# Optimization experiments

Hardware: AMD Instinct MI355X
Metric: run time of the kernel (lower is better)

Reference implementation:

```python
import jax, jax.numpy as jnp
import numpy as np
from jax import lax

# ---- geometry (from Mamba2PoSTMixer defaults + chosen d_model) ----
D_MODEL = 1024
EXPAND = 2
HEADDIM = 64
D_STATE = 128
D_CONV = 4
CHUNK = 256
D_INNER = EXPAND * D_MODEL            # 2048
NHEADS = D_INNER // HEADDIM           # 32
D_CONV_CH = D_INNER + 2 * D_STATE     # conv acts on x, B, C
D_IN_PROJ = 2 * D_INNER + 2 * D_STATE + NHEADS
BATCH, SEQLEN = 2, 4096
EPS = 1e-5


def setup_inputs() -> dict:
    key = jax.random.key(0)
    ks = jax.random.split(key, 8)
    f = jnp.float32
    return {
        "hidden_states": jax.random.normal(ks[0], (BATCH, SEQLEN, D_MODEL), f),
        "residual": jax.random.normal(ks[1], (BATCH, SEQLEN, D_MODEL), f),
        "norm_weight": jnp.ones((D_MODEL,), f),
        "in_proj_w": jax.random.normal(ks[2], (D_MODEL, D_IN_PROJ), f) * 0.02,
        "conv_w": jax.random.normal(ks[3], (D_CONV, 1, D_CONV_CH), f) * 0.2,  # WIO, depthwise
        "conv_b": jnp.zeros((D_CONV_CH,), f),
        "dt_bias": jnp.log(jnp.expm1(jax.random.uniform(ks[4], (NHEADS,), f, 1e-3, 1e-1))),
        "A_log": jnp.log(jax.random.uniform(ks[5], (NHEADS,), f, 1.0, 16.0)),
        "D": jnp.ones((NHEADS,), f),
        "gate_norm_weight": jnp.ones((D_INNER,), f),
        "out_proj_w": jax.random.normal(ks[6], (D_INNER, D_MODEL), f) * 0.02,
    }


def _rmsnorm(x, w, eps=EPS):
    return x * lax.rsqrt(jnp.mean(x * x, axis=-1, keepdims=True) + eps) * w


def _segsum(x):
    # x: [..., T] -> [..., T, T] lower-triangular cumulative segment sums
    T = x.shape[-1]
    cs = jnp.cumsum(x, axis=-1)
    ss = cs[..., :, None] - cs[..., None, :]
    mask = jnp.tril(jnp.ones((T, T), bool))
    return jnp.where(mask, ss, -jnp.inf)


def _ssd(xdt, dtA, Bm, Cm):
    # xdt: [b,l,h,p] (x already scaled by dt), dtA: [b,l,h], Bm/Cm: [b,l,n]
    b, l, h, p = xdt.shape
    n = Bm.shape[-1]
    c = l // CHUNK
    x = xdt.reshape(b, c, CHUNK, h, p)
    A = dtA.reshape(b, c, CHUNK, h).transpose(0, 3, 1, 2)     # [b,h,c,l]
    Bc = Bm.reshape(b, c, CHUNK, n)
    Cc = Cm.reshape(b, c, CHUNK, n)
    A_cum = jnp.cumsum(A, axis=-1)                            # [b,h,c,l]
    # intra-chunk (diagonal block) output
    L = jnp.exp(_segsum(A))                                   # [b,h,c,l,s]
    Y_diag = jnp.einsum('bcln,bcsn,bhcls,bcshp->bclhp', Cc, Bc, L, x)
    # per-chunk final states
    decay_states = jnp.exp(A_cum[..., -1:] - A_cum)           # [b,h,c,l]
    states = jnp.einsum('bcln,bhcl,bclhp->bchpn', Bc, decay_states, x)
    # inter-chunk recurrence over chunk states
    chunk_decay = jnp.exp(A_cum[..., -1])                     # [b,h,c]
    def step(carry, inp):
        dec, s = inp                                          # dec: [b,h], s: [b,h,p,n]
        return carry * dec[..., None, None] + s, carry
    init = jnp.zeros((b, h, p, n), xdt.dtype)
    _, prev = lax.scan(step, init,
                       (jnp.moveaxis(chunk_decay, -1, 0), jnp.moveaxis(states, 1, 0)))
    prev = jnp.moveaxis(prev, 0, 1)                           # [b,c,h,p,n] states entering each chunk
    Y_off = jnp.einsum('bcln,bchpn,bhcl->bclhp', Cc, prev, jnp.exp(A_cum))
    return (Y_diag + Y_off).reshape(b, l, h, p)


def reference(hidden_states, residual, norm_weight, in_proj_w, conv_w, conv_b,
              dt_bias, A_log, D, gate_norm_weight, out_proj_w):
    # residual add + RMSNorm (Mamba2PoSTBlock)
    res = hidden_states + residual
    h = _rmsnorm(res, norm_weight)
    # Mamba2 mixer
    zxbcdt = h @ in_proj_w                                    # [b,l, 2*Di + 2*N + H]
    z, xBC, dt_raw = jnp.split(zxbcdt, [D_INNER, D_INNER + D_CONV_CH], axis=-1)
    # depthwise causal conv over (x, B, C) channels + SiLU
    xp = jnp.pad(xBC, ((0, 0), (D_CONV - 1, 0), (0, 0)))
    xBC = lax.conv_general_dilated(xp, conv_w, (1,), 'VALID',
                                   dimension_numbers=('NWC', 'WIO', 'NWC'),
                                   feature_group_count=D_CONV_CH) + conv_b
    xBC = jax.nn.silu(xBC)
    x, Bm, Cm = jnp.split(xBC, [D_INNER, D_INNER + D_STATE], axis=-1)
    dt = jax.nn.softplus(dt_raw + dt_bias)                    # [b,l,H]
    A = -jnp.exp(A_log)                                       # [H]
    xh = x.reshape(x.shape[0], x.shape[1], NHEADS, HEADDIM)   # [b,l,h,p]
    y = _ssd(xh * dt[..., None], dt * A, Bm, Cm)
    y = y + D[None, None, :, None] * xh                       # skip (D) term
    y = y.reshape(y.shape[0], y.shape[1], D_INNER)
    y = _rmsnorm(y * jax.nn.silu(z), gate_norm_weight)        # gated RMSNorm
    out = y @ out_proj_w
    return out, res
```

## Files before the change

kernel.cpp:

```cpp
#include <hip/hip_runtime.h>
#include <hip/hip_bf16.h>
#include <math.h>

#define BATCH   2
#define LQ      4096
#define RTOT    8192
#define DM      1024
#define DI      2048
#define NH      32
#define HD      64
#define DS      128
#define CH      256
#define NC      16
#define XBC_C   2304
#define ZX_C    4384
#define ZXS     4352
#define NP1     4608
#define EPS     1e-5f
#define LOG2E   1.4426950408889634f

typedef __hip_bfloat16 bf16;
typedef __bf16 bf16x8v __attribute__((ext_vector_type(8)));
typedef __bf16 bf16x4v __attribute__((ext_vector_type(4)));
typedef float f32x4v __attribute__((ext_vector_type(4)));

__device__ __forceinline__ float block_reduce_sum(float v) {
    __shared__ float sred[8];
    int lane = threadIdx.x & 63, w = threadIdx.x >> 6;
#pragma unroll
    for (int off = 32; off > 0; off >>= 1) v += __shfl_down(v, off, 64);
    if (lane == 0) sred[w] = v;
    __syncthreads();
    float t = (threadIdx.x < (int)(blockDim.x >> 6)) ? sred[threadIdx.x] : 0.f;
    if (w == 0) {
#pragma unroll
        for (int off = 4; off > 0; off >>= 1) t += __shfl_down(t, off, 64);
        if (lane == 0) sred[0] = t;
    }
    __syncthreads();
    return sred[0];
}

__device__ __forceinline__ void transpose_tile(
    const float* __restrict__ W, bf16* __restrict__ WT, int K, int N,
    int n0, int k0) {
    __shared__ float t[32][33];
    int tx = threadIdx.x & 31, ty = threadIdx.x >> 5;
#pragma unroll
    for (int r = 0; r < 32; r += 8) {
        int k = k0 + ty + r, n = n0 + tx;
        t[ty + r][tx] = (n < N) ? W[(size_t)k * N + n] : 0.f;
    }
    __syncthreads();
#pragma unroll
    for (int r = 0; r < 32; r += 8) {
        int n = n0 + ty + r, k = k0 + tx;
        WT[(size_t)n * K + k] = __float2bfloat16(t[tx][ty + r]);
    }
}

__global__ __launch_bounds__(256) void fused_pre_kernel(
    const float* __restrict__ hid, const float* __restrict__ resid,
    const float* __restrict__ w, float* __restrict__ res_out,
    bf16* __restrict__ h_out, const float* __restrict__ in_proj,
    bf16* __restrict__ Bt1) {
    int bid = blockIdx.x;
    if (bid < RTOT) {
        int r = bid, tid = threadIdx.x;
        size_t base = (size_t)r * DM;
        float4 hv = *(const float4*)&hid[base + tid * 4];
        float4 rv = *(const float4*)&resid[base + tid * 4];
        float4 s = {hv.x + rv.x, hv.y + rv.y, hv.z + rv.z, hv.w + rv.w};
        *(float4*)&res_out[base + tid * 4] = s;
        float ss = s.x * s.x + s.y * s.y + s.z * s.z + s.w * s.w;
        ss = block_reduce_sum(ss);
        float scale = rsqrtf(ss / (float)DM + EPS);
        float4 wv = *(const float4*)&w[tid * 4];
        __hip_bfloat162 p0, p1;
        p0.x = __float2bfloat16(s.x * scale * wv.x);
        p0.y = __float2bfloat16(s.y * scale * wv.y);
        p1.x = __float2bfloat16(s.z * scale * wv.z);
        p1.y = __float2bfloat16(s.w * scale * wv.w);
        bf16* hp = &h_out[base + tid * 4];
        *(__hip_bfloat162*)hp = p0;
        *(__hip_bfloat162*)(hp + 2) = p1;
    } else {
        int t = bid - RTOT;
        transpose_tile(in_proj, Bt1, DM, ZX_C, (t % 144) * 32, (t / 144) * 32);
    }
}

#define GFENCE asm volatile("" ::: "memory")
#define GBAR do { GFENCE; __builtin_amdgcn_s_barrier(); GFENCE; } while (0)
#define GWAIT_LGKM                                                             \
    do {                                                                       \
        asm volatile("s_waitcnt lgkmcnt(0)" ::: "memory");                     \
        __builtin_amdgcn_sched_barrier(0);                                     \
    } while (0)
#define GWAIT_VM0 asm volatile("s_waitcnt vmcnt(0)" ::: "memory")
#define GWAIT_VMN                                                              \
    do {                                                                       \
        if constexpr (BN == 256)                                               \
            asm volatile("s_waitcnt vmcnt(6)" ::: "memory");                   \
        else                                                                   \
            asm volatile("s_waitcnt vmcnt(4)" ::: "memory");                   \
    } while (0)

#define RD_A(buf, ml)                                                          \
    do {                                                                       \
        _Pragma("unroll") for (int mt_ = 0; mt_ < 4; ++mt_)                    \
        _Pragma("unroll") for (int kk_ = 0; kk_ < 2; ++kk_)                    \
            aF[mt_][kk_] = *(const bf16x8v*)&As[buf][                          \
                (wm * 128 + ((ml) * 4 + mt_) * 16 + fr) * 64 +                 \
                ((((kk_ << 2) | kg) ^ s7) << 3)];                              \
    } while (0)

#define RD_B(buf)                                                              \
    do {                                                                       \
        _Pragma("unroll") for (int nt_ = 0; nt_ < NTW; ++nt_)                  \
        _Pragma("unroll") for (int kk_ = 0; kk_ < 2; ++kk_)                    \
            bF[nt_][kk_] = *(const bf16x8v*)&Bs[buf][                          \
                (wn * (BN / 4) + nt_ * 16 + fr) * 64 +                         \
                ((((kk_ << 2) | kg) ^ s7) << 3)];                              \
    } while (0)

#define QMFMA(ml, nl)                                                          \
    do {                                                                       \
        __builtin_amdgcn_s_setprio(1);                                         \
        _Pragma("unroll") for (int mt_ = 0; mt_ < 4; ++mt_)                    \
        _Pragma("unroll") for (int nt_ = 0; nt_ < NTH; ++nt_)                  \
        _Pragma("unroll") for (int kk_ = 0; kk_ < 2; ++kk_)                    \
            acc[(ml) * 4 + mt_][(nl) * NTH + nt_] =                            \
                __builtin_amdgcn_mfma_f32_16x16x32_bf16(                       \
                    aF[mt_][kk_], bF[(nl) * NTH + nt_][kk_],                   \
                    acc[(ml) * 4 + mt_][(nl) * NTH + nt_], 0, 0, 0);           \
        __builtin_amdgcn_s_setprio(0);                                         \
    } while (0)

template <int BN, int WRITE_F32>
__global__ __launch_bounds__(512, 2) void gemm_8ph_kernel(
    const bf16* __restrict__ A, int lda, const bf16* __restrict__ Bt, int ldb,
    void* __restrict__ C, int ldc, int NXT, int K, float* __restrict__ dtraw) {
    constexpr int BM = 256;
    constexpr int NTW = BN / 64;
    constexpr int NTH = NTW / 2;
    constexpr int BLOADS = BN / 128;
    __shared__ __align__(16) bf16 As[2][BM * 64];
    __shared__ __align__(16) bf16 Bs[2][BN * 64];

    const int tid = threadIdx.x;
    const int lane = tid & 63;
    const int wave = tid >> 6;
    const int wm = wave >> 2, wn = wave & 3;
    const int fr = lane & 15, kg = lane >> 4;
    const int s7 = fr & 7;

    const int bid = blockIdx.x;
    const int swz = (bid & 7) * ((int)gridDim.x >> 3) + (bid >> 3);
    const int mtile = swz / NXT;
    const int m0 = mtile * BM;
    const int n0 = (swz - mtile * NXT) * BN;

    const int trow = tid >> 3;
    const int scol = ((tid & 7) ^ (trow & 7)) << 3;
    const bf16* aSrc = A + (size_t)(m0 + trow) * lda + scol;
    const bf16* bSrc = Bt + (size_t)(n0 + trow) * ldb + scol;

    auto stageA = [&](int kt, int h) {
#pragma unroll
        for (int j = 0; j < 2; ++j)
            __builtin_amdgcn_global_load_lds(
                (const __attribute__((address_space(1))) void*)(
                    aSrc + (size_t)(h * 128 + j * 64) * lda + kt * 64),
                (__attribute__((address_space(3))) void*)(
                    &As[kt & 1][(h * 128 + j * 64) * 64 + tid * 8]),
                16, 0, 0);
    };
    auto stageB = [&](int kt, int h) {
#pragma unroll
        for (int j = 0; j < BLOADS; ++j)
            __builtin_amdgcn_global_load_lds(
                (const __attribute__((address_space(1))) void*)(
                    bSrc + (size_t)(h * (BN / 2) + j * 64) * ldb + kt * 64),
                (__attribute__((address_space(3))) void*)(
                    &Bs[kt & 1][(h * (BN / 2) + j * 64) * 64 + tid * 8]),
                16, 0, 0);
    };

    f32x4v acc[8][NTW] = {};
    bf16x8v aF[4][2], bF[NTW][2];

    stageB(0, 0); stageB(0, 1); stageA(0, 0); stageA(0, 1);
    stageB(1, 0); stageB(1, 1); stageA(1, 0);
    GWAIT_VMN;
    GBAR;

    const int NIT = K >> 7;
    for (int t = 0; t < NIT; ++t) {
        const int k1 = 2 * t + 1, k2 = 2 * t + 2, k3 = 2 * t + 3;
        const bool full = (t < NIT - 1);
        RD_B(0); RD_A(0, 0);
        stageA(k1, 1);
        GBAR; GWAIT_LGKM;
        QMFMA(0, 0);
        GBAR;
        if (full) stageB(k2, 0);
        GBAR;
        QMFMA(0, 1);
        GBAR;
        RD_A(0, 1);
        if (full) stageB(k2, 1);
        GBAR; GWAIT_LGKM;
        QMFMA(1, 0);
        GBAR;
        if (full) stageA(k2, 0);
        GBAR;
        QMFMA(1, 1);
        if (full) { GWAIT_VMN; } else { GWAIT_VM0; }
        GBAR;
        RD_B(1); RD_A(1, 0);
        if (full) stageA(k2, 1);
        GBAR; GWAIT_LGKM;
        QMFMA(0, 0);
        GBAR;
        if (full) stageB(k3, 0);
        GBAR;
        QMFMA(0, 1);
        GBAR;
        RD_A(1, 1);
        if (full) stageB(k3, 1);
        GBAR; GWAIT_LGKM;
        QMFMA(1, 0);
        GBAR;
        if (full) stageA(k3, 0);
        GBAR;
        QMFMA(1, 1);
        if (full) { GWAIT_VMN; }
        GBAR;
    }

#pragma unroll
    for (int mt = 0; mt < 8; ++mt) {
#pragma unroll
        for (int nt = 0; nt < NTW; ++nt) {
            int gn = n0 + wn * (BN / 4) + nt * 16 + fr;
#pragma unroll
            for (int rg = 0; rg < 4; ++rg) {
                int gm = m0 + wm * 128 + mt * 16 + kg * 4 + rg;
                float v = acc[mt][nt][rg];
                if (WRITE_F32) {
                    ((float*)C)[(size_t)gm * ldc + gn] = v;
                } else {
                    if (gn < 4352)
                        ((bf16*)C)[(size_t)gm * ldc + gn] = __float2bfloat16(v);
                    else if (gn < 4384)
                        dtraw[(size_t)gm * 32 + (gn - 4352)] = v;
                }
            }
        }
    }
}

__global__ __launch_bounds__(256) void fused_conv_dt_kernel(
    const bf16* __restrict__ zx, const float* __restrict__ conv_w,
    const float* __restrict__ conv_b, bf16* __restrict__ xBC,
    const float* __restrict__ dtraw, const float* __restrict__ dt_bias,
    const float* __restrict__ A_log, float* __restrict__ dt_bh,
    float* __restrict__ Ac2_bh) {
    int bid = blockIdx.x;
    if (bid < 9216) {
        int idx = bid * 256 + threadIdx.x;
        int r = idx / 288;
        int o = idx - r * 288;
        int c = o * 8;
        int b = r >> 12, l = r & (LQ - 1);
        float acc[8];
        {
            float4 cb0 = *(const float4*)&conv_b[c];
            float4 cb1 = *(const float4*)&conv_b[c + 4];
            acc[0] = cb0.x; acc[1] = cb0.y; acc[2] = cb0.z; acc[3] = cb0.w;
            acc[4] = cb1.x; acc[5] = cb1.y; acc[6] = cb1.z; acc[7] = cb1.w;
        }
#pragma unroll
        for (int k = 0; k < 4; ++k) {
            int t = l - 3 + k;
            if (t >= 0) {
                bf16x8v xv = *(const bf16x8v*)&zx[(size_t)(b * LQ + t) * ZXS + DI + c];
                float4 w0 = *(const float4*)&conv_w[k * XBC_C + c];
                float4 w1 = *(const float4*)&conv_w[k * XBC_C + c + 4];
                acc[0] = fmaf(w0.x, (float)xv[0], acc[0]);
                acc[1] = fmaf(w0.y, (float)xv[1], acc[1]);
                acc[2] = fmaf(w0.z, (float)xv[2], acc[2]);
                acc[3] = fmaf(w0.w, (float)xv[3], acc[3]);
                acc[4] = fmaf(w1.x, (float)xv[4], acc[4]);
                acc[5] = fmaf(w1.y, (float)xv[5], acc[5]);
                acc[6] = fmaf(w1.z, (float)xv[6], acc[6]);
                acc[7] = fmaf(w1.w, (float)xv[7], acc[7]);
            }
        }
        bf16x8v ov;
#pragma unroll
        for (int j = 0; j < 8; ++j)
            ov[j] = (__bf16)(acc[j] / (1.f + __expf(-acc[j])));
        *(bf16x8v*)&xBC[(size_t)r * XBC_C + c] = ov;
    } else {
        __shared__ float sA[256];
        int b2 = bid - 9216;
        int c = b2 & 15, h = (b2 >> 4) & 31, b = b2 >> 9;
        int tid = threadIdx.x;
        int l = c * CH + tid;
        int r = b * LQ + l;
        float v = dtraw[(size_t)r * 32 + h] + dt_bias[h];
        float dt = (v > 20.f) ? v : log1pf(expf(v));
        float A = -expf(A_log[h]);
        sA[tid] = dt * A * LOG2E;
        __syncthreads();
        for (int off = 1; off < 256; off <<= 1) {
            float t = (tid >= off) ? sA[tid - off] : 0.f;
            __syncthreads();
            sA[tid] += t;
            __syncthreads();
        }
        size_t o = (size_t)(b * NH + h) * LQ + l;
        dt_bh[o] = dt;
        Ac2_bh[o] = sA[tid];
    }
}

__global__ __launch_bounds__(256) void states_mfma_kernel(
    const bf16* __restrict__ xBC, const float* __restrict__ dt_bh,
    const float* __restrict__ Ac2, float* __restrict__ states) {
    __shared__ __align__(16) __bf16 xdT[64][264];
    __shared__ __align__(16) __bf16 BT[64][264];
    int bid = blockIdx.x;
    int c = bid & 15, h = (bid >> 4) & 31, b = bid >> 9;
    int bh = b * NH + h;
    int rch = b * LQ + c * CH;
    int tid = threadIdx.x;
    int wave = tid >> 6, lane = tid & 63;
    int fr = lane & 15, kg = lane >> 4;
    float Ac2last = Ac2[(size_t)bh * LQ + c * CH + (CH - 1)];

    {
        int p2 = (tid & 31) * 2;
        int srow = tid >> 5;
#pragma unroll 4
        for (int pass = 0; pass < 32; ++pass) {
            int s = pass * 8 + srow;
            float sc = dt_bh[(size_t)bh * LQ + c * CH + s] *
                       exp2f(Ac2last - Ac2[(size_t)bh * LQ + c * CH + s]);
            __hip_bfloat162 xv =
                *(const __hip_bfloat162*)&xBC[(size_t)(rch + s) * XBC_C + h * HD + p2];
            xdT[p2][s]     = (__bf16)(__bfloat162float(xv.x) * sc);
            xdT[p2 + 1][s] = (__bf16)(__bfloat162float(xv.y) * sc);
        }
    }
    int wm = (wave >> 1) * 32, wn = (wave & 1) * 32;
    size_t base = (size_t)(bh * NC + c) * HD * DS;
    for (int nh = 0; nh < 2; ++nh) {
        __syncthreads();
        {
            int n_oct = tid & 7, lrow = tid >> 3;
#pragma unroll
            for (int pass = 0; pass < 8; ++pass) {
                int l = pass * 32 + lrow;
                bf16x8v bv = *(const bf16x8v*)
                    &xBC[(size_t)(rch + l) * XBC_C + DI + nh * 64 + n_oct * 8];
#pragma unroll
                for (int j = 0; j < 8; ++j)
                    BT[n_oct * 8 + j][l] = bv[j];
            }
        }
        __syncthreads();
        f32x4v acc[2][2] = {};
#pragma unroll
        for (int kb = 0; kb < 8; ++kb) {
            bf16x8v A2[2], B2[2];
#pragma unroll
            for (int i = 0; i < 2; ++i)
                A2[i] = *(const bf16x8v*)&xdT[wm + i * 16 + fr][kb * 32 + kg * 8];
#pragma unroll
            for (int j = 0; j < 2; ++j)
                B2[j] = *(const bf16x8v*)&BT[wn + j * 16 + fr][kb * 32 + kg * 8];
#pragma unroll
            for (int i = 0; i < 2; ++i)
#pragma unroll
                for (int j = 0; j < 2; ++j)
                    acc[i][j] = __builtin_amdgcn_mfma_f32_16x16x32_bf16(
                        A2[i], B2[j], acc[i][j], 0, 0, 0);
        }
#pragma unroll
        for (int i = 0; i < 2; ++i)
#pragma unroll
            for (int j = 0; j < 2; ++j)
#pragma unroll
                for (int rg = 0; rg < 4; ++rg) {
                    int p = wm + i * 16 + kg * 4 + rg;
                    int n = nh * 64 + wn + j * 16 + fr;
                    states[base + (size_t)p * DS + n] = acc[i][j][rg];
                }
    }
}

__global__ __launch_bounds__(256) void chunk_scan_kernel(
    float* __restrict__ states, const float* __restrict__ Ac2) {
    int bh = blockIdx.x;
    int tid = threadIdx.x;
    float carry[32];
#pragma unroll
    for (int j = 0; j < 32; ++j) carry[j] = 0.f;
    for (int c = 0; c < NC; ++c) {
        float dec = exp2f(Ac2[(size_t)bh * LQ + c * CH + (CH - 1)]);
        size_t base = (size_t)(bh * NC + c) * (HD * DS);
#pragma unroll
        for (int j = 0; j < 32; ++j) {
            size_t idx = base + tid + j * 256;
            float tmp = states[idx];
            states[idx] = carry[j];
            carry[j] = carry[j] * dec + tmp;
        }
    }
}

template <int MASKED>
__device__ __forceinline__ void y_slab(
    const bf16* __restrict__ xBC, int rch, int s0, int fr, int kg,
    const float* As_sh, const float* Al, const bf16x8v CA[4][4],
    __bf16 (*Pw)[36], const __bf16 (*xdtT)[264], f32x4v accY[4][4]) {
#pragma unroll
    for (int half = 0; half < 2; ++half) {
        f32x4v Sacc[2][4] = {};
#pragma unroll
        for (int ks = 0; ks < 4; ++ks) {
            bf16x8v SB[2];
#pragma unroll
            for (int st2 = 0; st2 < 2; ++st2)
                SB[st2] = *(const bf16x8v*)&xBC[
                    (size_t)(rch + s0 + half * 32 + st2 * 16 + fr) * XBC_C
                    + DI + ks * 32 + kg * 8];
#pragma unroll
            for (int st2 = 0; st2 < 2; ++st2)
#pragma unroll
                for (int mt = 0; mt < 4; ++mt) {
                    if (MASKED && (half * 2 + st2) > mt) continue;
                    Sacc[st2][mt] = __builtin_amdgcn_mfma_f32_16x16x32_bf16(
                        SB[st2], CA[mt][ks], Sacc[st2][mt], 0, 0, 0);
                }
        }
#pragma unroll
        for (int st2 = 0; st2 < 2; ++st2) {
            int sblk = half * 2 + st2;
            float4 As4 = *(const float4*)&As_sh[s0 + half * 32 + st2 * 16 + kg * 4];
            float as[4] = {As4.x, As4.y, As4.z, As4.w};
#pragma unroll
            for (int mt = 0; mt < 4; ++mt) {
                bf16x4v pv;
                if (MASKED && sblk > mt) {
                    pv[0] = pv[1] = pv[2] = pv[3] = (__bf16)0.f;
                } else {
#pragma unroll
                    for (int rg = 0; rg < 4; ++rg) {
                        float v = Sacc[st2][mt][rg] * exp2f(Al[mt] - as[rg]);
                        if (MASKED && sblk == mt && (kg * 4 + rg) > fr) v = 0.f;
                        pv[rg] = (__bf16)v;
                    }
                }
                *(bf16x4v*)&Pw[mt * 16 + fr][st2 * 16 + kg * 4] = pv;
            }
        }
        __asm__ volatile("s_waitcnt lgkmcnt(0)" ::: "memory");
        bf16x8v PA[4], XB[4];
#pragma unroll
        for (int mt = 0; mt < 4; ++mt) {
            bf16x4v plo = *(const bf16x4v*)&Pw[mt * 16 + fr][kg * 8];
            bf16x4v phi = *(const bf16x4v*)&Pw[mt * 16 + fr][kg * 8 + 4];
            bf16x8v pa;
#pragma unroll
            for (int j = 0; j < 4; ++j) { pa[j] = plo[j]; pa[4 + j] = phi[j]; }
            PA[mt] = pa;
        }
#pragma unroll
        for (int pt = 0; pt < 4; ++pt)
            XB[pt] = *(const bf16x8v*)&xdtT[pt * 16 + fr][s0 + half * 32 + kg * 8];
#pragma unroll
        for (int mt = 0; mt < 4; ++mt)
#pragma unroll
            for (int pt = 0; pt < 4; ++pt)
                accY[mt][pt] = __builtin_amdgcn_mfma_f32_16x16x32_bf16(
                    PA[mt], XB[pt], accY[mt][pt], 0, 0, 0);
        __asm__ volatile("s_waitcnt lgkmcnt(0)" ::: "memory");
    }
}

__global__ __launch_bounds__(256) void y_mfma_kernel(
    const bf16* __restrict__ xBC, const float* __restrict__ dt_bh,
    const float* __restrict__ Ac2, const float* __restrict__ prev,
    bf16* __restrict__ yout ) {
    __shared__ __align__(16) __bf16 xdtT[64][264];
    __shared__ __align__(16) __bf16 P[4][64][36];
    __shared__ float As_sh[256];
    int bid = blockIdx.x;
    int c = bid & 15, h = (bid >> 4) & 31, b = bid >> 9;
    int bh = b * NH + h;
    int rch = b * LQ + c * CH;
    int tid = threadIdx.x;
    int wave = tid >> 6, lane = tid & 63;
    int fr = lane & 15, kg = lane >> 4;

    As_sh[tid] = Ac2[(size_t)bh * LQ + c * CH + tid];
    {
        int p2 = (tid & 31) * 2;
        int srow = tid >> 5;
#pragma unroll 4
        for (int pass = 0; pass < 32; ++pass) {
            int s = pass * 8 + srow;
            float dtv = dt_bh[(size_t)bh * LQ + c * CH + s];
            __hip_bfloat162 xv =
                *(const __hip_bfloat162*)&xBC[(size_t)(rch + s) * XBC_C + h * HD + p2];
            xdtT[p2][s]     = (__bf16)(__bfloat162float(xv.x) * dtv);
            xdtT[p2 + 1][s] = (__bf16)(__bfloat162float(xv.y) * dtv);
        }
    }
    __syncthreads();

    bf16x8v CA[4][4];
    {
        size_t rb = (size_t)(rch + wave * 64 + fr) * XBC_C + DI + DS + kg * 8;
#pragma unroll
        for (int mt = 0; mt < 4; ++mt)
#pragma unroll
            for (int ks = 0; ks < 4; ++ks)
                CA[mt][ks] = *(const bf16x8v*)&xBC[rb + (size_t)mt * 16 * XBC_C + ks * 32];
    }

    f32x4v accY[4][4] = {};

    {
        size_t pbase = (size_t)(bh * NC + c) * HD * DS;
#pragma unroll
        for (int ks = 0; ks < 4; ++ks) {
            bf16x8v PB[4];
#pragma unroll
            for (int pt = 0; pt < 4; ++pt) {
                const float* pp = &prev[pbase + (size_t)(pt * 16 + fr) * DS + ks * 32 + kg * 8];
                float4 a4 = *(const float4*)pp;
                float4 b4 = *(const float4*)(pp + 4);
                bf16x8v t;
                t[0] = (__bf16)a4.x; t[1] = (__bf16)a4.y; t[2] = (__bf16)a4.z; t[3] = (__bf16)a4.w;
                t[4] = (__bf16)b4.x; t[5] = (__bf16)b4.y; t[6] = (__bf16)b4.z; t[7] = (__bf16)b4.w;
                PB[pt] = t;
            }
#pragma unroll
            for (int mt = 0; mt < 4; ++mt)
#pragma unroll
                for (int pt = 0; pt < 4; ++pt)
                    accY[mt][pt] = __builtin_amdgcn_mfma_f32_16x16x32_bf16(
                        CA[mt][ks], PB[pt], accY[mt][pt], 0, 0, 0);
        }
    }
    int l0 = wave * 64;
#pragma unroll
    for (int mt = 0; mt < 4; ++mt) {
#pragma unroll
        for (int rg = 0; rg < 4; ++rg) {
            float e = exp2f(As_sh[l0 + mt * 16 + kg * 4 + rg]);
#pragma unroll
            for (int pt = 0; pt < 4; ++pt)
                accY[mt][pt][rg] *= e;
        }
    }

    float Al[4];
#pragma unroll
    for (int mt = 0; mt < 4; ++mt) Al[mt] = As_sh[l0 + mt * 16 + fr];

    __bf16 (*Pw)[36] = P[wave];
    for (int st = 0; st < wave; ++st)
        y_slab<0>(xBC, rch, st * 64, fr, kg, As_sh, Al, CA, Pw, xdtT, accY);
    y_slab<1>(xBC, rch, l0, fr, kg, As_sh, Al, CA, Pw, xdtT, accY);

#pragma unroll
    for (int ph = 0; ph < 2; ++ph) {
#pragma unroll
        for (int mt = 0; mt < 4; ++mt)
#pragma unroll
            for (int ptl = 0; ptl < 2; ++ptl)
#pragma unroll
                for (int rg = 0; rg < 4; ++rg)
                    Pw[mt * 16 + kg * 4 + rg][ptl * 16 + fr] =
                        (__bf16)accY[mt][ph * 2 + ptl][rg];
        __asm__ volatile("s_waitcnt lgkmcnt(0)" ::: "memory");
        bf16* yp = yout + (size_t)(rch + l0 + lane) * ZXS + h * HD + ph * 32;
#pragma unroll
        for (int q = 0; q < 4; ++q) {
            bf16x4v a = *(const bf16x4v*)&Pw[lane][q * 8];
            bf16x4v bq = *(const bf16x4v*)&Pw[lane][q * 8 + 4];
            bf16x8v v;
#pragma unroll
            for (int j = 0; j < 4; ++j) { v[j] = a[j]; v[4 + j] = bq[j]; }
            *(bf16x8v*)(yp + q * 8) = v;
        }
        __asm__ volatile("s_waitcnt lgkmcnt(0)" ::: "memory");
    }
}

__global__ __launch_bounds__(256) void fused_gate_trans_kernel(
    const bf16* __restrict__ zx, const float* __restrict__ gw,
    const float* __restrict__ Dvec, const bf16* __restrict__ xBC,
    bf16* __restrict__ y ,
    const float* __restrict__ out_proj, bf16* __restrict__ Bt2) {
    int bid = blockIdx.x;
    if (bid < RTOT) {
        int r = bid, tid = threadIdx.x;
        int i0 = tid * 8;
        bf16x8v zv = *(const bf16x8v*)&zx[(size_t)r * ZXS + i0];
        bf16x8v yv = *(const bf16x8v*)&y[(size_t)r * ZXS + i0];
        bf16x8v xv = *(const bf16x8v*)&xBC[(size_t)r * XBC_C + i0];
        float Dh = Dvec[tid >> 3];
        float v[8];
        float ss = 0.f;
#pragma unroll
        for (int j = 0; j < 8; ++j) {
            float z = (float)zv[j];
            float val = ((float)yv[j] + Dh * (float)xv[j]) * (z / (1.f + __expf(-z)));
            v[j] = val;
            ss += val * val;
        }
        ss = block_reduce_sum(ss);
        float scale = rsqrtf(ss / (float)DI + EPS);
        float4 g0 = *(const float4*)&gw[i0];
        float4 g1 = *(const float4*)&gw[i0 + 4];
        float g[8] = {g0.x, g0.y, g0.z, g0.w, g1.x, g1.y, g1.z, g1.w};
        bf16x8v ov;
#pragma unroll
        for (int j = 0; j < 8; ++j)
            ov[j] = (__bf16)(v[j] * scale * g[j]);
        *(bf16x8v*)&y[(size_t)r * ZXS + i0] = ov;
    } else {
        int t = bid - RTOT;
        transpose_tile(out_proj, Bt2, DI, DM, (t & 31) * 32, (t >> 5) * 32);
    }
}

extern "C" void kernel_launch(void* const* d_in, const int* in_sizes, int n_in,
                              void* d_out, int out_size, void* d_ws, size_t ws_size,
                              hipStream_t stream) {
    const float* hid      = (const float*)d_in[0];
    const float* resid    = (const float*)d_in[1];
    const float* norm_w   = (const float*)d_in[2];
    const float* in_proj  = (const float*)d_in[3];
    const float* conv_w   = (const float*)d_in[4];
    const float* conv_b   = (const float*)d_in[5];
    const float* dt_bias  = (const float*)d_in[6];
    const float* A_log    = (const float*)d_in[7];
    const float* Dvec     = (const float*)d_in[8];
    const float* gate_w   = (const float*)d_in[9];
    const float* out_proj = (const float*)d_in[10];

    float* out_p   = (float*)d_out;
    float* res_out = out_p + (size_t)RTOT * DM;
    bf16*  h_bf16  = (bf16*)out_p;
    float* states  = out_p;

    char* wsb = (char*)d_ws;
    bf16*  zx      = (bf16*)wsb;  wsb += (size_t)RTOT * ZXS * sizeof(bf16);
    bf16*  xBC     = (bf16*)wsb;  wsb += (size_t)RTOT * XBC_C * sizeof(bf16);
    float* dtraw   = (float*)wsb; wsb += (size_t)RTOT * 32 * sizeof(float);
    float* dt_bh   = (float*)wsb; wsb += (size_t)BATCH * NH * LQ * sizeof(float);
    float* Ac2_bh  = (float*)wsb; wsb += (size_t)BATCH * NH * LQ * sizeof(float);
    wsb += (size_t)1 << 20;
    bf16* Bt1 = xBC;
    bf16* Bt2 = (bf16*)dtraw;

    fused_pre_kernel<<<RTOT + 4608, 256, 0, stream>>>(
        hid, resid, norm_w, res_out, h_bf16, in_proj, Bt1);
    gemm_8ph_kernel<256, 0><<<576, 512, 0, stream>>>(
        h_bf16, DM, Bt1, DM, zx, ZXS, 18, DM, dtraw);
    fused_conv_dt_kernel<<<9216 + 1024, 256, 0, stream>>>(
        zx, conv_w, conv_b, xBC, dtraw, dt_bias, A_log, dt_bh, Ac2_bh);
    states_mfma_kernel<<<BATCH * NH * NC, 256, 0, stream>>>(
        xBC, dt_bh, Ac2_bh, states);
    chunk_scan_kernel<<<BATCH * NH, 256, 0, stream>>>(states, Ac2_bh);
    y_mfma_kernel<<<BATCH * NH * NC, 256, 0, stream>>>(
        xBC, dt_bh, Ac2_bh, states, zx + DI);
    fused_gate_trans_kernel<<<RTOT + 2048, 256, 0, stream>>>(
        zx, gate_w, Dvec, xBC, zx + DI, out_proj, Bt2);
    gemm_8ph_kernel<128, 1><<<256, 512, 0, stream>>>(
        zx + DI, ZXS, Bt2, DI, out_p, DM, 8, DI, nullptr);
}
```

Measured before the change: 498.9 us.

## Swizzle LDS transposes, split chunk scan across blocks, remap GEMM tiles per XCD

XOR-swizzles the column index of the transposed xdT/BT/xdtT shared-memory tiles so that MFMA fragment reads and the transposing writes avoid LDS bank conflicts. The chunk_scan kernel is split into 8 blocks per (batch, head), each handling a 1024-element slice, which raises parallelism from 64 blocks to 512. The GEMM block-to-tile mapping now gives each XCD a contiguous range of M tiles so blocks on the same XCD share A rows in L2. These are three independent changes; the swizzle must stay consistent across writers and readers.

```diff
diff --git a/kernel.cpp b/kernel.cpp
--- a/kernel.cpp
+++ b/kernel.cpp
@@ -23,6 +23,8 @@
 typedef __bf16 bf16x8v __attribute__((ext_vector_type(8)));
 typedef __bf16 bf16x4v __attribute__((ext_vector_type(4)));
 typedef float f32x4v __attribute__((ext_vector_type(4)));
+
+#define CSWZ(row, col) ((col) ^ ((((row) >> 3) & 7) << 3))
 
 __device__ __forceinline__ float block_reduce_sum(float v) {
     __shared__ float sred[8];
@@ -156,10 +158,12 @@
     const int s7 = fr & 7;
 
     const int bid = blockIdx.x;
-    const int swz = (bid & 7) * ((int)gridDim.x >> 3) + (bid >> 3);
-    const int mtile = swz / NXT;
+    const int xcd = bid & 7;
+    const int local = bid >> 3;
+    const int MPX = ((int)gridDim.x >> 3) / NXT;
+    const int mtile = xcd * MPX + (local % MPX);
     const int m0 = mtile * BM;
-    const int n0 = (swz - mtile * NXT) * BN;
+    const int n0 = (local / MPX) * BN;
 
     const int trow = tid >> 3;
     const int scol = ((tid & 7) ^ (trow & 7)) << 3;
@@ -344,6 +348,7 @@
     {
         int p2 = (tid & 31) * 2;
         int srow = tid >> 5;
+        int key = ((p2 >> 3) & 7) << 3;
 #pragma unroll 4
         for (int pass = 0; pass < 32; ++pass) {
             int s = pass * 8 + srow;
@@ -351,8 +356,9 @@
                        exp2f(Ac2last - Ac2[(size_t)bh * LQ + c * CH + s]);
             __hip_bfloat162 xv =
                 *(const __hip_bfloat162*)&xBC[(size_t)(rch + s) * XBC_C + h * HD + p2];
-            xdT[p2][s]     = (__bf16)(__bfloat162float(xv.x) * sc);
-            xdT[p2 + 1][s] = (__bf16)(__bfloat162float(xv.y) * sc);
+            int sx = s ^ key;
+            xdT[p2][sx]     = (__bf16)(__bfloat162float(xv.x) * sc);
+            xdT[p2 + 1][sx] = (__bf16)(__bfloat162float(xv.y) * sc);
         }
     }
     int wm = (wave >> 1) * 32, wn = (wave & 1) * 32;
@@ -364,11 +370,12 @@
 #pragma unroll
             for (int pass = 0; pass < 8; ++pass) {
                 int l = pass * 32 + lrow;
+                int lx = l ^ (n_oct << 3);
                 bf16x8v bv = *(const bf16x8v*)
                     &xBC[(size_t)(rch + l) * XBC_C + DI + nh * 64 + n_oct * 8];
 #pragma unroll
                 for (int j = 0; j < 8; ++j)
-                    BT[n_oct * 8 + j][l] = bv[j];
+                    BT[n_oct * 8 + j][lx] = bv[j];
             }
         }
         __syncthreads();
@@ -377,11 +384,15 @@
         for (int kb = 0; kb < 8; ++kb) {
             bf16x8v A2[2], B2[2];
 #pragma unroll
-            for (int i = 0; i < 2; ++i)
-                A2[i] = *(const bf16x8v*)&xdT[wm + i * 16 + fr][kb * 32 + kg * 8];
-#pragma unroll
-            for (int j = 0; j < 2; ++j)
-                B2[j] = *(const bf16x8v*)&BT[wn + j * 16 + fr][kb * 32 + kg * 8];
+            for (int i = 0; i < 2; ++i) {
+                int row = wm + i * 16 + fr;
+                A2[i] = *(const bf16x8v*)&xdT[row][CSWZ(row, kb * 32 + kg * 8)];
+            }
+#pragma unroll
+            for (int j = 0; j < 2; ++j) {
+                int row = wn + j * 16 + fr;
+                B2[j] = *(const bf16x8v*)&BT[row][CSWZ(row, kb * 32 + kg * 8)];
+            }
 #pragma unroll
             for (int i = 0; i < 2; ++i)
 #pragma unroll
@@ -404,16 +415,17 @@
 
 __global__ __launch_bounds__(256) void chunk_scan_kernel(
     float* __restrict__ states, const float* __restrict__ Ac2) {
-    int bh = blockIdx.x;
+    int bh = blockIdx.x >> 3;
+    int sl = blockIdx.x & 7;
     int tid = threadIdx.x;
-    float carry[32];
-#pragma unroll
-    for (int j = 0; j < 32; ++j) carry[j] = 0.f;
+    float carry[4];
+#pragma unroll
+    for (int j = 0; j < 4; ++j) carry[j] = 0.f;
     for (int c = 0; c < NC; ++c) {
         float dec = exp2f(Ac2[(size_t)bh * LQ + c * CH + (CH - 1)]);
-        size_t base = (size_t)(bh * NC + c) * (HD * DS);
-#pragma unroll
-        for (int j = 0; j < 32; ++j) {
+        size_t base = (size_t)(bh * NC + c) * (HD * DS) + sl * 1024;
+#pragma unroll
+        for (int j = 0; j < 4; ++j) {
             size_t idx = base + tid + j * 256;
             float tmp = states[idx];
             states[idx] = carry[j];
@@ -480,8 +492,11 @@
             PA[mt] = pa;
         }
 #pragma unroll
-        for (int pt = 0; pt < 4; ++pt)
-            XB[pt] = *(const bf16x8v*)&xdtT[pt * 16 + fr][s0 + half * 32 + kg * 8];
+        for (int pt = 0; pt < 4; ++pt) {
+            int row = pt * 16 + fr;
+            XB[pt] = *(const bf16x8v*)&xdtT[row][
+                CSWZ(row, s0 + half * 32 + kg * 8)];
+        }
 #pragma unroll
         for (int mt = 0; mt < 4; ++mt)
 #pragma unroll
@@ -511,14 +526,16 @@
     {
         int p2 = (tid & 31) * 2;
         int srow = tid >> 5;
+        int key = ((p2 >> 3) & 7) << 3;
 #pragma unroll 4
         for (int pass = 0; pass < 32; ++pass) {
             int s = pass * 8 + srow;
             float dtv = dt_bh[(size_t)bh * LQ + c * CH + s];
             __hip_bfloat162 xv =
                 *(const __hip_bfloat162*)&xBC[(size_t)(rch + s) * XBC_C + h * HD + p2];
-            xdtT[p2][s]     = (__bf16)(__bfloat162float(xv.x) * dtv);
-            xdtT[p2 + 1][s] = (__bf16)(__bfloat162float(xv.y) * dtv);
+            int sx = s ^ key;
+            xdtT[p2][sx]     = (__bf16)(__bfloat162float(xv.x) * dtv);
+            xdtT[p2 + 1][sx] = (__bf16)(__bfloat162float(xv.y) * dtv);
         }
     }
     __syncthreads();
@@ -680,7 +697,7 @@
         zx, conv_w, conv_b, xBC, dtraw, dt_bias, A_log, dt_bh, Ac2_bh);
     states_mfma_kernel<<<BATCH * NH * NC, 256, 0, stream>>>(
         xBC, dt_bh, Ac2_bh, states);
-    chunk_scan_kernel<<<BATCH * NH, 256, 0, stream>>>(states, Ac2_bh);
+    chunk_scan_kernel<<<BATCH * NH * 8, 256, 0, stream>>>(states, Ac2_bh);
     y_mfma_kernel<<<BATCH * NH * NC, 256, 0, stream>>>(
         xBC, dt_bh, Ac2_bh, states, zx + DI);
     fused_gate_trans_kernel<<<RTOT + 2048, 256, 0, stream>>>(
```

After: 486.8 us. 1.02x faster.
